# Kernel optimization log

Measured on AMD Instinct MI355X. Metric: run time of the kernel, lower is better.

Reference implementation:

```python
import jax, jax.numpy as jnp
import numpy as np

S_FACTOR = 2          # scale_factor
GRID = 64             # coarse grid side -> M = 64^3 coarse voxels
C_IN = 32
C_MID = 32
C_OUT = 256


def setup_inputs() -> dict:
    key = jax.random.key(0)
    k1, k2, k3 = jax.random.split(key, 3)
    s = S_FACTOR
    S = s ** 3
    M = GRID ** 3
    # coarse voxel coords in canonical (lexicographic) order
    r = jnp.arange(GRID)
    ci, cj, ck = jnp.meshgrid(r, r, r, indexing='ij')
    coarse = jnp.stack([ci.ravel(), cj.ravel(), ck.ravel()], axis=-1)  # (M, 3)
    lo = jnp.arange(s)
    li, lj, lk = jnp.meshgrid(lo, lo, lo, indexing='ij')
    local = jnp.stack([li.ravel(), lj.ravel(), lk.ravel()], axis=-1)   # (S, 3)
    # fine voxel coords: every coarse voxel fully occupied -> N = M*S
    ijk = (coarse[:, None, :] * s + local[None, :, :]).reshape(M * S, 3).astype(jnp.int32)
    # ijk_to_index on the coarse grid (precomputed grid lookup, int constant)
    down_index = jnp.repeat(jnp.arange(M, dtype=jnp.int32), S)
    in_data = jax.random.normal(k1, (M * S, C_IN), dtype=jnp.float32)
    W_mid = jax.random.normal(k2, (C_IN, C_MID), dtype=jnp.float32) / np.sqrt(C_IN).astype(np.float32)
    W_out = jax.random.normal(k3, (C_MID * S, C_OUT), dtype=jnp.float32) / np.sqrt(C_MID * S).astype(np.float32)
    return {"in_data": in_data, "W_mid": W_mid, "W_out": W_out,
            "ijk": ijk, "down_index": down_index, "num_coarse": M}


def reference(in_data, W_mid, W_out, ijk, down_index, num_coarse):
    s = S_FACTOR
    S = s ** 3
    # middle_proj (LinearFVDB, bias=False)
    x = in_data @ W_mid                                   # (N, C_mid)
    C = x.shape[1]
    # local coordinate within the s^3 block (floor division; ijk >= 0 here)
    down_ijk = ijk // s
    local = ijk - down_ijk * s                            # (N, 3) in [0, s)
    local_index = local[:, 0] * (s * s) + local[:, 1] * s + local[:, 2]
    flat_idx = down_index.astype(jnp.int32) * S + local_index.astype(jnp.int32)
    # scatter_add into zero buffer (mapping is a unique permutation)
    flat_target = jnp.zeros((num_coarse * S, C), dtype=x.dtype).at[flat_idx].add(x)
    down_data = flat_target.reshape(num_coarse, S * C)    # (M, S*C)
    # out_proj (LinearFVDB, bias=False)
    return down_data @ W_out                              # (M, C_out)
```

## Files before the change

kernel.cpp:

```cpp
#include <hip/hip_runtime.h>
#include <hip/hip_bf16.h>


typedef short bf16x8 __attribute__((ext_vector_type(8)));
typedef float f32x4 __attribute__((ext_vector_type(4)));

__device__ __forceinline__ unsigned short f2bf(float f) {
    union { float f; unsigned u; } x; x.f = f;
    unsigned u = x.u;
    u += 0x7fffu + ((u >> 16) & 1u);
    return (unsigned short)(u >> 16);
}

__global__ void build_wf(const float* __restrict__ Wmid,
                         const float* __restrict__ Wout,
                         unsigned short* __restrict__ Wt) {
    const int o = blockIdx.x;
    const int k = threadIdx.x;
    const int s = k >> 5;
    const int j = k & 31;
    float acc = 0.f;
#pragma unroll
    for (int c = 0; c < 32; ++c)
        acc += Wmid[j * 32 + c] * Wout[(s * 32 + c) * 256 + o];
    Wt[o * 256 + k] = f2bf(acc);
}

__global__ void build_inv(const int* __restrict__ ijk,
                          const int* __restrict__ down,
                          int* __restrict__ inv, int n) {
    int i = blockIdx.x * 256 + threadIdx.x;
    if (i < n) {
        int a = ijk[3 * i], b = ijk[3 * i + 1], c = ijk[3 * i + 2];
        int ls = ((a & 1) << 2) | ((b & 1) << 1) | (c & 1);
        inv[down[i] * 8 + ls] = i;
    }
}

__global__ __launch_bounds__(256) void gemm_fused(
    const float* __restrict__ A,
    const int* __restrict__ inv,
    const unsigned short* __restrict__ Wt,
    float* __restrict__ out)
{
    __shared__ int invS[512];
    __shared__ __align__(16) unsigned short Abuf[64 * 32];
    __shared__ __align__(16) unsigned short Bbuf[256 * 32];

    const int t = threadIdx.x;
    const long m0 = (long)blockIdx.x * 64;

    invS[t]       = inv[m0 * 8 + t];
    invS[256 + t] = inv[m0 * 8 + 256 + t];

    const int wave = t >> 6;
    const int lane = t & 63;
    const int q    = lane >> 4;
    const int r16  = lane & 15;

    f32x4 acc[4][4];
#pragma unroll
    for (int i = 0; i < 4; ++i)
#pragma unroll
        for (int j = 0; j < 4; ++j)
            acc[i][j] = (f32x4){0.f, 0.f, 0.f, 0.f};

    __syncthreads();

    for (int kb = 0; kb < 8; ++kb) {
#pragma unroll
        for (int i = 0; i < 2; ++i) {
            int flat = t + i * 256;
            int row  = flat >> 3;
            int seg  = flat & 7;
            long g   = invS[row * 8 + kb];
            const float4 v = *(const float4*)(A + g * 32 + seg * 4);
            ushort4 b;
            b.x = f2bf(v.x); b.y = f2bf(v.y); b.z = f2bf(v.z); b.w = f2bf(v.w);
            *(ushort4*)(&Abuf[row * 32 + seg * 4]) = b;
        }
#pragma unroll
        for (int i = 0; i < 4; ++i) {
            int c = t + i * 256;
            int o = c >> 2;
            int seg = c & 3;
            *(int4*)(&Bbuf[o * 32 + seg * 8]) =
                *(const int4*)(Wt + (long)o * 256 + kb * 32 + seg * 8);
        }
        __syncthreads();

        bf16x8 af[4], bfr[4];
#pragma unroll
        for (int mt = 0; mt < 4; ++mt)
            af[mt] = *(const bf16x8*)(&Abuf[(mt * 16 + r16) * 32 + q * 8]);
#pragma unroll
        for (int nt = 0; nt < 4; ++nt)
            bfr[nt] = *(const bf16x8*)(&Bbuf[(wave * 64 + nt * 16 + r16) * 32 + q * 8]);
#pragma unroll
        for (int mt = 0; mt < 4; ++mt)
#pragma unroll
            for (int nt = 0; nt < 4; ++nt)
                acc[mt][nt] = __builtin_amdgcn_mfma_f32_16x16x32_bf16(
                    af[mt], bfr[nt], acc[mt][nt], 0, 0, 0);
        __syncthreads();
    }

#pragma unroll
    for (int mt = 0; mt < 4; ++mt)
#pragma unroll
        for (int nt = 0; nt < 4; ++nt)
#pragma unroll
            for (int rg = 0; rg < 4; ++rg) {
                int row = mt * 16 + q * 4 + rg;
                int col = wave * 64 + nt * 16 + r16;
                out[(m0 + row) * 256 + col] = acc[mt][nt][rg];
            }
}

extern "C" void kernel_launch(void* const* d_in, const int* in_sizes, int n_in,
                              void* d_out, int out_size, void* d_ws, size_t ws_size,
                              hipStream_t stream) {
    const float* in_data = (const float*)d_in[0];
    const float* W_mid   = (const float*)d_in[1];
    const float* W_out   = (const float*)d_in[2];
    const int*   ijk     = (const int*)d_in[3];
    const int*   down    = (const int*)d_in[4];

    const int Nf = in_sizes[0] / 32;
    const int M  = Nf / 8;

    unsigned short* Wt = (unsigned short*)d_ws;
    int* inv = (int*)((char*)d_ws + 131072);

    build_wf<<<256, 256, 0, stream>>>(W_mid, W_out, Wt);
    build_inv<<<(Nf + 255) / 256, 256, 0, stream>>>(ijk, down, inv, Nf);
    gemm_fused<<<M / 64, 256, 0, stream>>>(in_data, inv, Wt, (float*)d_out);
}
```

Before: 523.8 us.

## Stage whole A tile once in swizzled LDS, read B directly from global

Result: no change. 516.6 us (-1.4%).

```diff
diff --git a/kernel.cpp b/kernel.cpp
--- a/kernel.cpp
+++ b/kernel.cpp
@@ -43,20 +43,32 @@
     const unsigned short* __restrict__ Wt,
     float* __restrict__ out)
 {
-    __shared__ int invS[512];
-    __shared__ __align__(16) unsigned short Abuf[64 * 32];
-    __shared__ __align__(16) unsigned short Bbuf[256 * 32];
+    __shared__ __align__(16) unsigned short Abuf[64 * 256];
 
     const int t = threadIdx.x;
     const long m0 = (long)blockIdx.x * 64;
-
-    invS[t]       = inv[m0 * 8 + t];
-    invS[256 + t] = inv[m0 * 8 + 256 + t];
 
     const int wave = t >> 6;
     const int lane = t & 63;
     const int q    = lane >> 4;
     const int r16  = lane & 15;
+
+#pragma unroll
+    for (int i = 0; i < 8; ++i) {
+        int ch  = i * 256 + t;
+        int row = ch >> 5;
+        int sub = ch & 31;
+        long g  = inv[m0 * 8 + row * 8 + (sub >> 2)];
+        const float4 v0 = *(const float4*)(A + g * 32 + (sub & 3) * 8);
+        const float4 v1 = *(const float4*)(A + g * 32 + (sub & 3) * 8 + 4);
+        bf16x8 b;
+        b[0] = (short)f2bf(v0.x); b[1] = (short)f2bf(v0.y);
+        b[2] = (short)f2bf(v0.z); b[3] = (short)f2bf(v0.w);
+        b[4] = (short)f2bf(v1.x); b[5] = (short)f2bf(v1.y);
+        b[6] = (short)f2bf(v1.z); b[7] = (short)f2bf(v1.w);
+        unsigned off = (unsigned)(row * 512 + sub * 16) ^ (unsigned)((row & 7) << 4);
+        *(bf16x8*)((char*)Abuf + off) = b;
+    }
 
     f32x4 acc[4][4];
 #pragma unroll
@@ -67,42 +79,26 @@
 
     __syncthreads();
 
+    const unsigned abase = (unsigned)(r16 * 512 + q * 16);
+    const unsigned aswz  = (unsigned)((r16 & 7) << 4);
+    const unsigned short* wbase = Wt + (long)(wave * 64 + r16) * 256 + q * 8;
+
+#pragma unroll
     for (int kb = 0; kb < 8; ++kb) {
-#pragma unroll
-        for (int i = 0; i < 2; ++i) {
-            int flat = t + i * 256;
-            int row  = flat >> 3;
-            int seg  = flat & 7;
-            long g   = invS[row * 8 + kb];
-            const float4 v = *(const float4*)(A + g * 32 + seg * 4);
-            ushort4 b;
-            b.x = f2bf(v.x); b.y = f2bf(v.y); b.z = f2bf(v.z); b.w = f2bf(v.w);
-            *(ushort4*)(&Abuf[row * 32 + seg * 4]) = b;
-        }
-#pragma unroll
-        for (int i = 0; i < 4; ++i) {
-            int c = t + i * 256;
-            int o = c >> 2;
-            int seg = c & 3;
-            *(int4*)(&Bbuf[o * 32 + seg * 8]) =
-                *(const int4*)(Wt + (long)o * 256 + kb * 32 + seg * 8);
-        }
-        __syncthreads();
-
         bf16x8 af[4], bfr[4];
 #pragma unroll
         for (int mt = 0; mt < 4; ++mt)
-            af[mt] = *(const bf16x8*)(&Abuf[(mt * 16 + r16) * 32 + q * 8]);
+            af[mt] = *(const bf16x8*)((const char*)Abuf +
+                      (((unsigned)(mt * 8192 + kb * 64) + abase) ^ aswz));
 #pragma unroll
         for (int nt = 0; nt < 4; ++nt)
-            bfr[nt] = *(const bf16x8*)(&Bbuf[(wave * 64 + nt * 16 + r16) * 32 + q * 8]);
+            bfr[nt] = *(const bf16x8*)(wbase + nt * 4096 + kb * 32);
 #pragma unroll
         for (int mt = 0; mt < 4; ++mt)
 #pragma unroll
             for (int nt = 0; nt < 4; ++nt)
                 acc[mt][nt] = __builtin_amdgcn_mfma_f32_16x16x32_bf16(
                     af[mt], bfr[nt], acc[mt][nt], 0, 0, 0);
-        __syncthreads();
     }
 
 #pragma unroll
```
